# Performance work log

Measured on AMD Instinct MI355X. Metric: run time of the kernel, lower is better.

## Reference

```python
import jax, jax.numpy as jnp
import numpy as np

P = 100_000      # distinct products
T = 300_000      # total product nodes after repeat_interleave (sum of cnt)
NQ = 100_000     # query nodes
B = 8192         # number of sessions (segments)
QIN = 128; PIN = 128; D = 128; MSL = 50; DL = D - MSL


def setup_inputs() -> dict:
    key = jax.random.key(0)
    ks = jax.random.split(key, 12)
    # irregular repeat counts in {1..5}, tiled so sum == 3*P == T exactly (static shape)
    cnt = jnp.asarray(np.tile(np.array([1, 2, 3, 4, 5], np.int32), P // 5))
    s = 0.05
    return {
        "query_feat": jax.random.normal(ks[0], (NQ, QIN), jnp.float32),
        "product_feat": jax.random.normal(ks[1], (P, PIN), jnp.float32),
        "Wq": jax.random.normal(ks[2], (DL, QIN), jnp.float32) * s,
        "bq": jnp.zeros((DL,), jnp.float32),
        "Wp": jax.random.normal(ks[3], (DL, PIN), jnp.float32) * s,
        "bp": jnp.zeros((DL,), jnp.float32),
        "pos_table": jax.random.normal(ks[4], (MSL, MSL), jnp.float32) * s,
        "Wn": jax.random.normal(ks[5], (D, D), jnp.float32) * s,
        "bn": jnp.zeros((D,), jnp.float32),
        "Wc": jax.random.normal(ks[6], (D, D), jnp.float32) * s,
        "Wa": jax.random.normal(ks[7], (1, D), jnp.float32) * s,
        "query_pos_id": jax.random.randint(ks[8], (NQ,), 0, MSL, jnp.int32),
        "product_pos_id": jax.random.randint(ks[9], (T,), 0, MSL, jnp.int32),
        "query_batch": jax.random.randint(ks[10], (NQ,), 0, B, jnp.int32),
        "product_batch": jax.random.randint(ks[11], (P,), 0, B, jnp.int32),
        "cnt": cnt,
        "num_segments": B,
        "total_product_nodes": T,
    }


def _segment_mean(x, seg, num_segments):
    sums = jax.ops.segment_sum(x, seg, num_segments=num_segments)
    counts = jax.ops.segment_sum(jnp.ones((x.shape[0],), x.dtype), seg, num_segments=num_segments)
    return sums / jnp.maximum(counts, 1.0)[:, None]


def reference(query_feat, product_feat, Wq, bq, Wp, bp, pos_table, Wn, bn, Wc, Wa,
              query_pos_id, product_pos_id, query_batch, product_batch, cnt,
              num_segments, total_product_nodes):
    # query branch: linear -> concat positional embedding -> tanh  [NQ, D]
    qe = jnp.tanh(jnp.concatenate([query_feat @ Wq.T + bq, pos_table[query_pos_id]], axis=1))
    # product branch: linear, repeat_interleave by cnt, concat pos emb, tanh  [T, D]
    pe = product_feat @ Wp.T + bp
    pe = jnp.repeat(pe, cnt, axis=0, total_repeat_length=total_product_nodes)
    pe = jnp.tanh(jnp.concatenate([pe, pos_table[product_pos_id]], axis=1))
    pbatch = jnp.repeat(product_batch, cnt, axis=0, total_repeat_length=total_product_nodes)
    # stack nodes (products first, then queries — matches torch.concat order)
    node_emb = jnp.concatenate([pe, qe], axis=0)            # [N, D]
    node_batch = jnp.concatenate([pbatch, query_batch], axis=0)
    # coarse session representation: segment mean, broadcast back to nodes
    coarse = _segment_mean(node_emb, node_batch, num_segments)  # [B, D]
    coarse_g = coarse[node_batch]                                # [N, D]
    # attention gating
    att = jax.nn.sigmoid(node_emb @ Wn.T + bn + coarse_g @ Wc.T) @ Wa.T  # [N, 1]
    weighted = node_emb * att
    return _segment_mean(weighted, node_batch, num_segments)    # [B, D]
```

## Files before the change

kernel.cpp:

```cpp
#include <hip/hip_runtime.h>
#include <hip/hip_bf16.h>
#include <math.h>


constexpr int D   = 128;
constexpr int DL  = 78;
constexpr int MSL = 50;
constexpr int RP  = 80;

typedef __attribute__((ext_vector_type(8))) short bfrag8;
typedef __attribute__((ext_vector_type(4))) float facc4;
typedef __attribute__((ext_vector_type(4))) short short4v;

__device__ __forceinline__ float sigmoidf_(float x) {
    return 1.f / (1.f + __expf(-x));
}
__device__ __forceinline__ float ftanh(float x) {
    float e = __expf(2.f * x);
    return 1.f - 2.f * __builtin_amdgcn_rcpf(e + 1.f);
}

__device__ __forceinline__ char* ldsAddr(__hip_bfloat16* base, int row, int byte_in_row) {
    return reinterpret_cast<char*>(base) + row * 256 + (byte_in_row ^ ((row & 7) << 4));
}
__device__ __forceinline__ bfrag8 ldsR16(const __hip_bfloat16* base, int row, int byte_in_row) {
    return *reinterpret_cast<const bfrag8*>(
        reinterpret_cast<const char*>(base) + row * 256 + (byte_in_row ^ ((row & 7) << 4)));
}
__device__ __forceinline__ short4v ldsR8(const __hip_bfloat16* base, int row, int byte_in_row) {
    return *reinterpret_cast<const short4v*>(
        reinterpret_cast<const char*>(base) + row * 256 + (byte_in_row ^ ((row & 7) << 4)));
}

__device__ __forceinline__ bfrag8 cvt8(float4 a, float4 b) {
    __hip_bfloat16 t[8] = {__float2bfloat16(a.x), __float2bfloat16(a.y),
                           __float2bfloat16(a.z), __float2bfloat16(a.w),
                           __float2bfloat16(b.x), __float2bfloat16(b.y),
                           __float2bfloat16(b.z), __float2bfloat16(b.w)};
    return *reinterpret_cast<bfrag8*>(t);
}

__global__ __launch_bounds__(256) void k_tables2(
    const float* __restrict__ pos_table, const float* __restrict__ Wn,
    float* __restrict__ tpos, float* __restrict__ posWn) {
    __shared__ float tposL[MSL * MSL];
    int t = threadIdx.x;
    for (int o = t; o < MSL * MSL; o += 256) tposL[o] = tanhf(pos_table[o]);
    __syncthreads();
    if (blockIdx.x == 0)
        for (int o = t; o < MSL * MSL; o += 256) tpos[o] = tposL[o];
    for (int o = blockIdx.x * 256 + t; o < MSL * D; o += gridDim.x * 256) {
        int r = o >> 7, d = o & 127;
        float acc = 0.f;
        #pragma unroll 10
        for (int j = 0; j < MSL; ++j) acc += tposL[r * MSL + j] * Wn[d * D + DL + j];
        posWn[o] = acc;
    }
}

__global__ __launch_bounds__(256) void k_convW(
    const float* __restrict__ Wq, const float* __restrict__ Wp, const float* __restrict__ Wn,
    __hip_bfloat16* __restrict__ Wqbf, __hip_bfloat16* __restrict__ Wpbf,
    __hip_bfloat16* __restrict__ Wnbf) {
    int i = blockIdx.x * 256 + threadIdx.x;
    if (i < 80 * 128) {
        int n = i >> 7;
        Wqbf[i] = __float2bfloat16((n < DL) ? Wq[i] : 0.f);
        Wpbf[i] = __float2bfloat16((n < DL) ? Wp[i] : 0.f);
    } else if (i < 80 * 128 + 128 * 128) {
        int o = i - 80 * 128;
        int j = o & 127;
        Wnbf[o] = __float2bfloat16((j < DL) ? Wn[o] : 0.f);
    }
}

__global__ void k_scanA(const int* __restrict__ cnt, int P, int* __restrict__ chunkSum) {
    __shared__ int s[256];
    int p = blockIdx.x * 256 + threadIdx.x;
    s[threadIdx.x] = (p < P) ? cnt[p] : 0;
    __syncthreads();
    for (int st = 128; st > 0; st >>= 1) {
        if (threadIdx.x < st) s[threadIdx.x] += s[threadIdx.x + st];
        __syncthreads();
    }
    if (threadIdx.x == 0) chunkSum[blockIdx.x] = s[0];
}
__global__ __launch_bounds__(1024) void k_scanB(
    const int* __restrict__ chunkSum, int nC, int* __restrict__ chunkOff) {
    __shared__ int s[1024];
    int t = threadIdx.x;
    int carry = 0;
    for (int base = 0; base < nC; base += 1024) {
        int v = (base + t < nC) ? chunkSum[base + t] : 0;
        s[t] = v;
        __syncthreads();
        for (int st = 1; st < 1024; st <<= 1) {
            int add = (t >= st) ? s[t - st] : 0;
            __syncthreads();
            s[t] += add;
            __syncthreads();
        }
        if (base + t < nC) chunkOff[base + t] = carry + s[t] - v;
        carry += s[1023];
        __syncthreads();
    }
}
__global__ void k_scanC(const int* __restrict__ cnt, int P, const int* __restrict__ chunkOff,
                        int* __restrict__ prodOff) {
    __shared__ int s[256];
    int t = threadIdx.x;
    int p = blockIdx.x * 256 + t;
    int v = (p < P) ? cnt[p] : 0;
    s[t] = v;
    __syncthreads();
    for (int st = 1; st < 256; st <<= 1) {
        int add = (t >= st) ? s[t - st] : 0;
        __syncthreads();
        s[t] += add;
        __syncthreads();
    }
    if (p < P) prodOff[p] = chunkOff[blockIdx.x] + s[t] - v;
}

__global__ void k_nodecnt(const int* __restrict__ qbatch, const int* __restrict__ pbatch,
                          int NQ, int N, int* __restrict__ nodeCnt) {
    int r = blockIdx.x * 256 + threadIdx.x;
    if (r >= N) return;
    int b = (r < NQ) ? qbatch[r] : pbatch[r - NQ];
    atomicAdd(&nodeCnt[b], 1);
}
__global__ __launch_bounds__(1024) void k_scanSeg(
    const int* __restrict__ nodeCnt, int B, int* __restrict__ segOff, int* __restrict__ cursor) {
    __shared__ int s[1024];
    int t = threadIdx.x;
    int carry = 0;
    for (int base = 0; base < B; base += 1024) {
        int v = (base + t < B) ? nodeCnt[base + t] : 0;
        s[t] = v;
        __syncthreads();
        for (int st = 1; st < 1024; st <<= 1) {
            int add = (t >= st) ? s[t - st] : 0;
            __syncthreads();
            s[t] += add;
            __syncthreads();
        }
        if (base + t < B) {
            int e = carry + s[t] - v;
            segOff[base + t] = e;
            cursor[base + t] = e;
        }
        carry += s[1023];
        __syncthreads();
    }
    if (t == 0) segOff[B] = carry;
}
__global__ void k_rank(const int* __restrict__ qbatch, const int* __restrict__ pbatch,
                       int NQ, int N, int* __restrict__ cursor, int* __restrict__ rowOf) {
    int r = blockIdx.x * 256 + threadIdx.x;
    if (r >= N) return;
    int b = (r < NQ) ? qbatch[r] : pbatch[r - NQ];
    int slot = atomicAdd(&cursor[b], 1);
    rowOf[slot] = r;
}

__global__ __launch_bounds__(256) void k_branch2(
    const float* __restrict__ qfeat, const float* __restrict__ pfeat,
    const __hip_bfloat16* __restrict__ Wqbf, const __hip_bfloat16* __restrict__ Wpbf,
    const float* __restrict__ bq, const float* __restrict__ bp,
    const __hip_bfloat16* __restrict__ Wnbf,
    const int* __restrict__ qbatch, const int* __restrict__ pbatch,
    const int* __restrict__ qpos, const int* __restrict__ ppos,
    const int* __restrict__ cnt, const int* __restrict__ prodOff,
    int NQ, int P, int qBlocks,
    __hip_bfloat16* __restrict__ tq, __hip_bfloat16* __restrict__ tp,
    __hip_bfloat16* __restrict__ qWn, __hip_bfloat16* __restrict__ pWn,
    int* __restrict__ hist) {
    const bool isQ = (int)blockIdx.x < qBlocks;
    const int r0 = (isQ ? blockIdx.x : blockIdx.x - qBlocks) * 64;
    const float* feat = isQ ? qfeat : pfeat;
    const __hip_bfloat16* Wbf = isQ ? Wqbf : Wpbf;
    const float* bias = isQ ? bq : bp;
    const int* batch = isQ ? qbatch : pbatch;
    const int Nrows = isQ ? NQ : P;
    __hip_bfloat16* tE  = isQ ? tq : tp;
    __hip_bfloat16* eWn = isQ ? qWn : pWn;

    __shared__ __hip_bfloat16 linL[64 * 128];
    __shared__ __hip_bfloat16 eWnL[64 * 128];
    int t = threadIdx.x;
    int l = t & 63, w = t >> 6;
    int lr = l & 15, lq = l >> 4;
    int am = w * 16 + lr;

    if (l < 16) {
        bfrag8 z = {0, 0, 0, 0, 0, 0, 0, 0};
        *reinterpret_cast<bfrag8*>(ldsAddr(linL, w * 16 + l, 160)) = z;
        *reinterpret_cast<bfrag8*>(ldsAddr(linL, w * 16 + l, 176)) = z;
    }

    int gra = r0 + am;
    const float* frow = &feat[(size_t)(gra < Nrows ? gra : Nrows - 1) * 128];
    bfrag8 a[4];
    #pragma unroll
    for (int kt = 0; kt < 4; ++kt) {
        float4 u = *reinterpret_cast<const float4*>(&frow[kt * 32 + lq * 8]);
        float4 v = *reinterpret_cast<const float4*>(&frow[kt * 32 + lq * 8 + 4]);
        a[kt] = cvt8(u, v);
    }

    facc4 c1[5];
    #pragma unroll
    for (int nt = 0; nt < 5; ++nt) { facc4 z = {0.f, 0.f, 0.f, 0.f}; c1[nt] = z; }
    #pragma unroll
    for (int nt = 0; nt < 5; ++nt) {
        #pragma unroll
        for (int kt = 0; kt < 4; ++kt) {
            bfrag8 b = *reinterpret_cast<const bfrag8*>(&Wbf[(nt * 16 + lr) * 128 + kt * 32 + lq * 8]);
            c1[nt] = __builtin_amdgcn_mfma_f32_16x16x32_bf16(a[kt], b, c1[nt], 0, 0, 0);
        }
    }

    #pragma unroll
    for (int nt = 0; nt < 5; ++nt) {
        int n = nt * 16 + lr;
        float bs = (n < DL) ? bias[n] : 0.f;
        #pragma unroll
        for (int j = 0; j < 4; ++j) {
            int m = w * 16 + lq * 4 + j;
            float tv = (n < DL) ? ftanh(c1[nt][j] + bs) : 0.f;
            *reinterpret_cast<__hip_bfloat16*>(ldsAddr(linL, m, 2 * n)) = __float2bfloat16(tv);
        }
    }

    {
        int r = w * 16 + (l >> 2), c = l & 3;
        int gr = r0 + r;
        #pragma unroll
        for (int j = 0; j < 5; ++j) {
            short4v v = ldsR8(linL, r, c * 40 + j * 8);
            if (gr < Nrows)
                *reinterpret_cast<short4v*>(&tE[(size_t)gr * RP + c * 20 + j * 4]) = v;
        }
    }

    bfrag8 a2[3];
    #pragma unroll
    for (int kt = 0; kt < 3; ++kt) a2[kt] = ldsR16(linL, am, kt * 64 + lq * 16);
    facc4 c2[8];
    #pragma unroll
    for (int nt = 0; nt < 8; ++nt) { facc4 z = {0.f, 0.f, 0.f, 0.f}; c2[nt] = z; }
    #pragma unroll
    for (int nt = 0; nt < 8; ++nt) {
        #pragma unroll
        for (int kt = 0; kt < 3; ++kt) {
            bfrag8 b = *reinterpret_cast<const bfrag8*>(&Wnbf[(nt * 16 + lr) * 128 + kt * 32 + lq * 8]);
            c2[nt] = __builtin_amdgcn_mfma_f32_16x16x32_bf16(a2[kt], b, c2[nt], 0, 0, 0);
        }
    }
    #pragma unroll
    for (int nt = 0; nt < 8; ++nt) {
        int d2 = nt * 16 + lr;
        #pragma unroll
        for (int j = 0; j < 4; ++j) {
            int m = w * 16 + lq * 4 + j;
            *reinterpret_cast<__hip_bfloat16*>(ldsAddr(eWnL, m, 2 * d2)) =
                __float2bfloat16(c2[nt][j]);
        }
    }
    {
        int r = w * 16 + (l >> 2), c = l & 3;
        int gr = r0 + r;
        #pragma unroll
        for (int j = 0; j < 4; ++j) {
            bfrag8 v = ldsR16(eWnL, r, c * 64 + j * 16);
            if (gr < Nrows)
                *reinterpret_cast<bfrag8*>(&eWn[(size_t)gr * 128 + c * 32 + j * 8]) = v;
        }
    }

    if (t < 64) {
        int gr = r0 + t;
        if (gr < Nrows) {
            int b = batch[gr];
            if (isQ) {
                atomicAdd(&hist[b * MSL + qpos[gr]], 1);
            } else {
                int c = cnt[gr], off2 = prodOff[gr];
                for (int j = 0; j < c; ++j)
                    atomicAdd(&hist[b * MSL + ppos[off2 + j]], 1);
            }
        }
    }
}

__global__ __launch_bounds__(128) void k_segsum2(
    const __hip_bfloat16* __restrict__ tq, const __hip_bfloat16* __restrict__ tp,
    const int* __restrict__ cnt, const int* __restrict__ rowOf,
    const int* __restrict__ segOff, const int* __restrict__ hist,
    const float* __restrict__ tpos, int NQ,
    float* __restrict__ segsum, float* __restrict__ segcnt) {
    int b = blockIdx.x, t = threadIdx.x;
    if (t < DL) {
        int s0 = segOff[b], s1 = segOff[b + 1];
        float acc = 0.f;
        for (int i = s0; i < s1; ++i) {
            int r = rowOf[i];
            float wv, val;
            if (r < NQ) {
                wv = 1.f;
                val = __bfloat162float(tq[(size_t)r * RP + t]);
            } else {
                int pr = r - NQ;
                wv = (float)cnt[pr];
                val = __bfloat162float(tp[(size_t)pr * RP + t]);
            }
            acc += wv * val;
        }
        segsum[(size_t)b * D + t] = acc;
    } else {
        int k = t - DL;
        float acc = 0.f, c = 0.f;
        for (int r = 0; r < MSL; ++r) {
            float h = (float)hist[b * MSL + r];
            acc += h * tpos[r * MSL + k];
            c += h;
        }
        segsum[(size_t)b * D + DL + k] = acc;
        if (k == 0) segcnt[b] = c;
    }
}

__global__ __launch_bounds__(256) void k_coarse(
    const float* __restrict__ segsum, const float* __restrict__ segcnt,
    const float* __restrict__ Wc, const float* __restrict__ bn, int B,
    float* __restrict__ coarseWc) {
    __shared__ __hip_bfloat16 WcL[128 * 130];
    __shared__ float cL[16 * 128];
    int t = threadIdx.x;
    int b0 = blockIdx.x * 16;
    for (int o = t; o < D * D; o += 256) {
        int d = o >> 7, k = o & 127;
        WcL[d * 130 + k] = __float2bfloat16(Wc[o]);
    }
    for (int o = t; o < 16 * D; o += 256) {
        int bb = o >> 7, d = o & 127;
        int b = b0 + bb;
        cL[o] = (b < B) ? segsum[(size_t)b * D + d] / fmaxf(segcnt[b], 1.f) : 0.f;
    }
    __syncthreads();
    for (int o = t; o < 16 * D; o += 256) {
        int bb = o >> 7, d = o & 127;
        int b = b0 + bb;
        if (b >= B) continue;
        float acc = bn[d];
        const float* cr = &cL[bb * 128];
        const __hip_bfloat16* wr = &WcL[d * 130];
        #pragma unroll 8
        for (int j = 0; j < D; ++j) acc += cr[j] * __bfloat162float(wr[j]);
        coarseWc[(size_t)b * D + d] = acc;
    }
}

__global__ __launch_bounds__(256) void k_att(
    const __hip_bfloat16* __restrict__ pWn, const __hip_bfloat16* __restrict__ tp,
    const __hip_bfloat16* __restrict__ qWn, const __hip_bfloat16* __restrict__ tq,
    const float* __restrict__ coarseWc, const float* __restrict__ posWn,
    const float* __restrict__ tpos, const float* __restrict__ Wa,
    const int* __restrict__ pbatch, const int* __restrict__ qbatch,
    const int* __restrict__ prodOff, const int* __restrict__ cnt,
    const int* __restrict__ ppos, const int* __restrict__ qpos,
    int P, int NQ, int pBlocks, float* __restrict__ out) {
    int wv = threadIdx.x >> 6, l = threadIdx.x & 63;
    if ((int)blockIdx.x < pBlocks) {
        int p = blockIdx.x * 4 + wv;
        if (p >= P) return;
        int b = pbatch[p], off = prodOff[p], c = cnt[p];
        float base0 = __bfloat162float(pWn[(size_t)p * D + l])      + coarseWc[(size_t)b * D + l];
        float base1 = __bfloat162float(pWn[(size_t)p * D + 64 + l]) + coarseWc[(size_t)b * D + 64 + l];
        float wa0 = Wa[l], wa1 = Wa[64 + l];
        float part[5];
        int   posr[5];
        #pragma unroll
        for (int j = 0; j < 5; ++j) {
            bool on = j < c;
            int pos = on ? ppos[off + j] : 0;
            posr[j] = pos;
            float z0 = base0 + posWn[pos * D + l];
            float z1 = base1 + posWn[pos * D + 64 + l];
            part[j] = on ? (sigmoidf_(z0) * wa0 + sigmoidf_(z1) * wa1) : 0.f;
        }
        #pragma unroll
        for (int m = 1; m < 64; m <<= 1) {
            #pragma unroll
            for (int j = 0; j < 5; ++j) part[j] += __shfl_xor(part[j], m, 64);
        }
        float attsum = part[0] + part[1] + part[2] + part[3] + part[4];
        float posacc = 0.f;
        if (l >= 14) {
            #pragma unroll
            for (int j = 0; j < 5; ++j)
                posacc += part[j] * tpos[posr[j] * MSL + (l - 14)];
        }
        float t0 = __bfloat162float(tp[(size_t)p * RP + l]);
        atomicAdd(&out[(size_t)b * D + l], attsum * t0);
        if (l < 14) {
            float t1 = __bfloat162float(tp[(size_t)p * RP + 64 + l]);
            atomicAdd(&out[(size_t)b * D + 64 + l], attsum * t1);
        } else {
            atomicAdd(&out[(size_t)b * D + 64 + l], posacc);
        }
    } else {
        int q = (blockIdx.x - pBlocks) * 4 + wv;
        if (q >= NQ) return;
        int b = qbatch[q], pos = qpos[q];
        float z0 = __bfloat162float(qWn[(size_t)q * D + l])      + coarseWc[(size_t)b * D + l]      + posWn[pos * D + l];
        float z1 = __bfloat162float(qWn[(size_t)q * D + 64 + l]) + coarseWc[(size_t)b * D + 64 + l] + posWn[pos * D + 64 + l];
        float part = sigmoidf_(z0) * Wa[l] + sigmoidf_(z1) * Wa[64 + l];
        #pragma unroll
        for (int m = 1; m < 64; m <<= 1) part += __shfl_xor(part, m, 64);
        float e0 = __bfloat162float(tq[(size_t)q * RP + l]);
        atomicAdd(&out[(size_t)b * D + l], part * e0);
        float e1 = (l < 14) ? __bfloat162float(tq[(size_t)q * RP + 64 + l]) : tpos[pos * MSL + (l - 14)];
        atomicAdd(&out[(size_t)b * D + 64 + l], part * e1);
    }
}

__global__ void k_final(float* __restrict__ out, const float* __restrict__ segcnt, int B) {
    int i = blockIdx.x * 256 + threadIdx.x;
    if (i < B * D) out[i] = out[i] / fmaxf(segcnt[i >> 7], 1.f);
}

extern "C" void kernel_launch(void* const* d_in, const int* in_sizes, int n_in,
                              void* d_out, int out_size, void* d_ws, size_t ws_size,
                              hipStream_t stream) {
    const float* query_feat   = (const float*)d_in[0];
    const float* product_feat = (const float*)d_in[1];
    const float* Wq = (const float*)d_in[2];
    const float* bq = (const float*)d_in[3];
    const float* Wp = (const float*)d_in[4];
    const float* bp = (const float*)d_in[5];
    const float* pos_table = (const float*)d_in[6];
    const float* Wn = (const float*)d_in[7];
    const float* bn = (const float*)d_in[8];
    const float* Wc = (const float*)d_in[9];
    const float* Wa = (const float*)d_in[10];
    const int* qpos   = (const int*)d_in[11];
    const int* ppos   = (const int*)d_in[12];
    const int* qbatch = (const int*)d_in[13];
    const int* pbatch = (const int*)d_in[14];
    const int* cnt    = (const int*)d_in[15];

    int NQ = in_sizes[11];
    int P  = in_sizes[15];
    int B  = out_size / D;
    int N  = NQ + P;
    float* out = (float*)d_out;

    char* w = (char*)d_ws;
    size_t off = 0;
    auto take = [&](size_t bytes) -> char* {
        char* p = w + off;
        off = (off + bytes + 255) & ~(size_t)255;
        return p;
    };
    float* segsum  = (float*)take((size_t)B * D * 4);
    int*   hist    = (int*)  take((size_t)B * MSL * 4);
    int*   nodeCnt = (int*)  take((size_t)B * 4);
    size_t zeroBytes = off;
    float* segcnt   = (float*)take((size_t)B * 4);
    float* coarseWc = (float*)take((size_t)B * D * 4);
    float* tpos  = (float*)take(MSL * MSL * 4);
    float* posWn = (float*)take(MSL * D * 4);
    __hip_bfloat16* Wqbf = (__hip_bfloat16*)take(80 * 128 * 2);
    __hip_bfloat16* Wpbf = (__hip_bfloat16*)take(80 * 128 * 2);
    __hip_bfloat16* Wnbf = (__hip_bfloat16*)take(128 * 128 * 2);
    int nC = (P + 255) / 256;
    int* chunkSum = (int*)take((size_t)nC * 4);
    int* chunkOff = (int*)take((size_t)nC * 4);
    int* prodOff  = (int*)take((size_t)P * 4);
    int* segOffA  = (int*)take((size_t)(B + 1) * 4);
    int* cursor   = (int*)take((size_t)B * 4);
    int* rowOf    = (int*)take((size_t)N * 4);
    __hip_bfloat16* tq  = (__hip_bfloat16*)take((size_t)NQ * RP * 2);
    __hip_bfloat16* tp  = (__hip_bfloat16*)take((size_t)P * RP * 2);
    __hip_bfloat16* qWn = (__hip_bfloat16*)take((size_t)NQ * D * 2);
    __hip_bfloat16* pWn = (__hip_bfloat16*)take((size_t)P * D * 2);
    (void)ws_size; (void)n_in;

    hipMemsetAsync(segsum, 0, zeroBytes, stream);
    hipMemsetAsync(out, 0, (size_t)out_size * 4, stream);

    hipLaunchKernelGGL(k_tables2, dim3(8), dim3(256), 0, stream, pos_table, Wn, tpos, posWn);
    hipLaunchKernelGGL(k_convW, dim3((80 * 128 + 128 * 128 + 255) / 256), dim3(256), 0, stream,
                       Wq, Wp, Wn, Wqbf, Wpbf, Wnbf);
    hipLaunchKernelGGL(k_scanA, dim3(nC), dim3(256), 0, stream, cnt, P, chunkSum);
    hipLaunchKernelGGL(k_scanB, dim3(1), dim3(1024), 0, stream, chunkSum, nC, chunkOff);
    hipLaunchKernelGGL(k_scanC, dim3(nC), dim3(256), 0, stream, cnt, P, chunkOff, prodOff);

    hipLaunchKernelGGL(k_nodecnt, dim3((N + 255) / 256), dim3(256), 0, stream,
                       qbatch, pbatch, NQ, N, nodeCnt);
    hipLaunchKernelGGL(k_scanSeg, dim3(1), dim3(1024), 0, stream, nodeCnt, B, segOffA, cursor);
    hipLaunchKernelGGL(k_rank, dim3((N + 255) / 256), dim3(256), 0, stream,
                       qbatch, pbatch, NQ, N, cursor, rowOf);

    int qBlocks = (NQ + 63) / 64, pBlocksBr = (P + 63) / 64;
    hipLaunchKernelGGL(k_branch2, dim3(qBlocks + pBlocksBr), dim3(256), 0, stream,
                       query_feat, product_feat, Wqbf, Wpbf, bq, bp, Wnbf,
                       qbatch, pbatch, qpos, ppos, cnt, prodOff, NQ, P, qBlocks,
                       tq, tp, qWn, pWn, hist);

    hipLaunchKernelGGL(k_segsum2, dim3(B), dim3(128), 0, stream,
                       tq, tp, cnt, rowOf, segOffA, hist, tpos, NQ, segsum, segcnt);
    hipLaunchKernelGGL(k_coarse, dim3((B + 15) / 16), dim3(256), 0, stream,
                       segsum, segcnt, Wc, bn, B, coarseWc);

    int pBlocksAtt = (P + 3) / 4, qBlocksAtt = (NQ + 3) / 4;
    hipLaunchKernelGGL(k_att, dim3(pBlocksAtt + qBlocksAtt), dim3(256), 0, stream,
                       pWn, tp, qWn, tq, coarseWc, posWn, tpos, Wa,
                       pbatch, qbatch, prodOff, cnt, ppos, qpos, P, NQ, pBlocksAtt, out);
    hipLaunchKernelGGL(k_final, dim3((B * D + 255) / 256), dim3(256), 0, stream, out, segcnt, B);
}
```

Measured before the change: 329.7 us.

## Restructure attention pass to per-segment waves, removing atomics and final divide

The attention kernel now assigns one wavefront per session segment and walks that segment's nodes through the precomputed rowOf/segOff CSR ordering. Each wave accumulates its result in registers and writes the normalized output directly, which removes per-node global atomics, the output memset and the separate k_final launch. The trade-off is less parallelism: only B/4 blocks are launched, and each wave loops serially over a variable number of nodes, so segment-length imbalance and reduced occupancy may hurt. The segsum memset is also dropped by reordering workspace allocation, which relies on k_segsum2 writing segsum fully.

After: 316.8 us. 1.04x faster.

```diff
diff --git a/kernel.cpp b/kernel.cpp
--- a/kernel.cpp
+++ b/kernel.cpp
@@ -361,73 +361,73 @@
     }
 }
 
-__global__ __launch_bounds__(256) void k_att(
+__global__ __launch_bounds__(256) void k_att3(
     const __hip_bfloat16* __restrict__ pWn, const __hip_bfloat16* __restrict__ tp,
     const __hip_bfloat16* __restrict__ qWn, const __hip_bfloat16* __restrict__ tq,
     const float* __restrict__ coarseWc, const float* __restrict__ posWn,
     const float* __restrict__ tpos, const float* __restrict__ Wa,
-    const int* __restrict__ pbatch, const int* __restrict__ qbatch,
+    const int* __restrict__ rowOf, const int* __restrict__ segOff,
     const int* __restrict__ prodOff, const int* __restrict__ cnt,
     const int* __restrict__ ppos, const int* __restrict__ qpos,
-    int P, int NQ, int pBlocks, float* __restrict__ out) {
+    const float* __restrict__ segcnt, int NQ, int B,
+    float* __restrict__ out) {
     int wv = threadIdx.x >> 6, l = threadIdx.x & 63;
-    if ((int)blockIdx.x < pBlocks) {
-        int p = blockIdx.x * 4 + wv;
-        if (p >= P) return;
-        int b = pbatch[p], off = prodOff[p], c = cnt[p];
-        float base0 = __bfloat162float(pWn[(size_t)p * D + l])      + coarseWc[(size_t)b * D + l];
-        float base1 = __bfloat162float(pWn[(size_t)p * D + 64 + l]) + coarseWc[(size_t)b * D + 64 + l];
-        float wa0 = Wa[l], wa1 = Wa[64 + l];
-        float part[5];
-        int   posr[5];
-        #pragma unroll
-        for (int j = 0; j < 5; ++j) {
-            bool on = j < c;
-            int pos = on ? ppos[off + j] : 0;
-            posr[j] = pos;
-            float z0 = base0 + posWn[pos * D + l];
-            float z1 = base1 + posWn[pos * D + 64 + l];
-            part[j] = on ? (sigmoidf_(z0) * wa0 + sigmoidf_(z1) * wa1) : 0.f;
-        }
-        #pragma unroll
-        for (int m = 1; m < 64; m <<= 1) {
+    int b = blockIdx.x * 4 + wv;
+    if (b >= B) return;
+
+    float cw0 = coarseWc[(size_t)b * D + l];
+    float cw1 = coarseWc[(size_t)b * D + 64 + l];
+    float wa0 = Wa[l], wa1 = Wa[64 + l];
+    float acc0 = 0.f, acc1 = 0.f, posacc = 0.f;
+    int s0 = segOff[b], s1 = segOff[b + 1];
+
+    for (int i = s0; i < s1; ++i) {
+        int r = rowOf[i];
+        if (r < NQ) {
+            int pos = qpos[r];
+            float z0 = __bfloat162float(qWn[(size_t)r * D + l])      + cw0 + posWn[pos * D + l];
+            float z1 = __bfloat162float(qWn[(size_t)r * D + 64 + l]) + cw1 + posWn[pos * D + 64 + l];
+            float part = sigmoidf_(z0) * wa0 + sigmoidf_(z1) * wa1;
             #pragma unroll
-            for (int j = 0; j < 5; ++j) part[j] += __shfl_xor(part[j], m, 64);
-        }
-        float attsum = part[0] + part[1] + part[2] + part[3] + part[4];
-        float posacc = 0.f;
-        if (l >= 14) {
+            for (int m = 1; m < 64; m <<= 1) part += __shfl_xor(part, m, 64);
+            acc0 += part * __bfloat162float(tq[(size_t)r * RP + l]);
+            if (l < 14) acc1 += part * __bfloat162float(tq[(size_t)r * RP + 64 + l]);
+            else posacc += part * tpos[pos * MSL + (l - 14)];
+        } else {
+            int p = r - NQ;
+            int off = prodOff[p], c = cnt[p];
+            float base0 = __bfloat162float(pWn[(size_t)p * D + l])      + cw0;
+            float base1 = __bfloat162float(pWn[(size_t)p * D + 64 + l]) + cw1;
+            float part[5];
+            int   posr[5];
             #pragma unroll
-            for (int j = 0; j < 5; ++j)
-                posacc += part[j] * tpos[posr[j] * MSL + (l - 14)];
-        }
-        float t0 = __bfloat162float(tp[(size_t)p * RP + l]);
-        atomicAdd(&out[(size_t)b * D + l], attsum * t0);
-        if (l < 14) {
-            float t1 = __bfloat162float(tp[(size_t)p * RP + 64 + l]);
-            atomicAdd(&out[(size_t)b * D + 64 + l], attsum * t1);
-        } else {
-            atomicAdd(&out[(size_t)b * D + 64 + l], posacc);
-        }
-    } else {
-        int q = (blockIdx.x - pBlocks) * 4 + wv;
-        if (q >= NQ) return;
-        int b = qbatch[q], pos = qpos[q];
-        float z0 = __bfloat162float(qWn[(size_t)q * D + l])      + coarseWc[(size_t)b * D + l]      + posWn[pos * D + l];
-        float z1 = __bfloat162float(qWn[(size_t)q * D + 64 + l]) + coarseWc[(size_t)b * D + 64 + l] + posWn[pos * D + 64 + l];
-        float part = sigmoidf_(z0) * Wa[l] + sigmoidf_(z1) * Wa[64 + l];
-        #pragma unroll
-        for (int m = 1; m < 64; m <<= 1) part += __shfl_xor(part, m, 64);
-        float e0 = __bfloat162float(tq[(size_t)q * RP + l]);
-        atomicAdd(&out[(size_t)b * D + l], part * e0);
-        float e1 = (l < 14) ? __bfloat162float(tq[(size_t)q * RP + 64 + l]) : tpos[pos * MSL + (l - 14)];
-        atomicAdd(&out[(size_t)b * D + 64 + l], part * e1);
-    }
-}
-
-__global__ void k_final(float* __restrict__ out, const float* __restrict__ segcnt, int B) {
-    int i = blockIdx.x * 256 + threadIdx.x;
-    if (i < B * D) out[i] = out[i] / fmaxf(segcnt[i >> 7], 1.f);
+            for (int j = 0; j < 5; ++j) {
+                bool on = j < c;
+                int pos = on ? ppos[off + j] : 0;
+                posr[j] = pos;
+                float z0 = base0 + posWn[pos * D + l];
+                float z1 = base1 + posWn[pos * D + 64 + l];
+                part[j] = on ? (sigmoidf_(z0) * wa0 + sigmoidf_(z1) * wa1) : 0.f;
+            }
+            #pragma unroll
+            for (int m = 1; m < 64; m <<= 1) {
+                #pragma unroll
+                for (int j = 0; j < 5; ++j) part[j] += __shfl_xor(part[j], m, 64);
+            }
+            float attsum = part[0] + part[1] + part[2] + part[3] + part[4];
+            if (l >= 14) {
+                #pragma unroll
+                for (int j = 0; j < 5; ++j)
+                    posacc += part[j] * tpos[posr[j] * MSL + (l - 14)];
+            }
+            acc0 += attsum * __bfloat162float(tp[(size_t)p * RP + l]);
+            if (l < 14) acc1 += attsum * __bfloat162float(tp[(size_t)p * RP + 64 + l]);
+        }
+    }
+
+    float inv = 1.f / fmaxf(segcnt[b], 1.f);
+    out[(size_t)b * D + l] = acc0 * inv;
+    out[(size_t)b * D + 64 + l] = (l < 14 ? acc1 : posacc) * inv;
 }
 
 extern "C" void kernel_launch(void* const* d_in, const int* in_sizes, int n_in,
@@ -463,10 +463,10 @@
         off = (off + bytes + 255) & ~(size_t)255;
         return p;
     };
-    float* segsum  = (float*)take((size_t)B * D * 4);
     int*   hist    = (int*)  take((size_t)B * MSL * 4);
     int*   nodeCnt = (int*)  take((size_t)B * 4);
     size_t zeroBytes = off;
+    float* segsum  = (float*)take((size_t)B * D * 4);
     float* segcnt   = (float*)take((size_t)B * 4);
     float* coarseWc = (float*)take((size_t)B * D * 4);
     float* tpos  = (float*)take(MSL * MSL * 4);
@@ -487,8 +487,7 @@
     __hip_bfloat16* pWn = (__hip_bfloat16*)take((size_t)P * D * 2);
     (void)ws_size; (void)n_in;
 
-    hipMemsetAsync(segsum, 0, zeroBytes, stream);
-    hipMemsetAsync(out, 0, (size_t)out_size * 4, stream);
+    hipMemsetAsync(hist, 0, zeroBytes, stream);
 
     hipLaunchKernelGGL(k_tables2, dim3(8), dim3(256), 0, stream, pos_table, Wn, tpos, posWn);
     hipLaunchKernelGGL(k_convW, dim3((80 * 128 + 128 * 128 + 255) / 256), dim3(256), 0, stream,
@@ -514,9 +513,7 @@
     hipLaunchKernelGGL(k_coarse, dim3((B + 15) / 16), dim3(256), 0, stream,
                        segsum, segcnt, Wc, bn, B, coarseWc);
 
-    int pBlocksAtt = (P + 3) / 4, qBlocksAtt = (NQ + 3) / 4;
-    hipLaunchKernelGGL(k_att, dim3(pBlocksAtt + qBlocksAtt), dim3(256), 0, stream,
+    hipLaunchKernelGGL(k_att3, dim3((B + 3) / 4), dim3(256), 0, stream,
                        pWn, tp, qWn, tq, coarseWc, posWn, tpos, Wa,
-                       pbatch, qbatch, prodOff, cnt, ppos, qpos, P, NQ, pBlocksAtt, out);
-    hipLaunchKernelGGL(k_final, dim3((B * D + 255) / 256), dim3(256), 0, stream, out, segcnt, B);
-}
+                       rowOf, segOffA, prodOff, cnt, ppos, qpos, segcnt, NQ, B, out);
+}
```
